# Kernel tuning notes

Hardware: AMD Instinct MI355X
Metric: run time of the kernel (lower is better)

## Reference

```python
import jax, jax.numpy as jnp
import numpy as np

B, N, C, O, K = 8, 1024, 64, 64, 3  # batch, nodes, in_c, out_c, Cheb order
EPS = 1e-12


def setup_inputs() -> dict:
    key = jax.random.key(0)
    ks = jax.random.split(key, 10)
    X_real = jax.random.normal(ks[0], (B, N, C), dtype=jnp.float32)
    X_imag = jax.random.normal(ks[1], (B, N, C), dtype=jnp.float32)
    L_real = jax.random.normal(ks[2], (B, K + 1, N, N), dtype=jnp.float32)
    L_imag = jax.random.normal(ks[3], (B, K + 1, N, N), dtype=jnp.float32)
    # Chebyshev weights: uniform(-stdv, stdv) then normalized to unit complex magnitude (as in __init__)
    stdv = 1.0 / np.sqrt(O)
    w_real = jax.random.uniform(ks[4], (K + 1, C, O), minval=-stdv, maxval=stdv, dtype=jnp.float32)
    w_imag = jax.random.uniform(ks[5], (K + 1, C, O), minval=-stdv, maxval=stdv, dtype=jnp.float32)
    mag = jnp.sqrt(w_real ** 2 + w_imag ** 2)
    w_real = w_real / mag
    w_imag = w_imag / mag
    # complex attention linear: maps 2*C -> 1
    a_stdv = 1.0 / np.sqrt(2 * C)
    attn_w_real = jax.random.uniform(ks[6], (2 * C,), minval=-a_stdv, maxval=a_stdv, dtype=jnp.float32)
    attn_w_imag = jax.random.uniform(ks[7], (2 * C,), minval=-a_stdv, maxval=a_stdv, dtype=jnp.float32)
    attn_b_real = jnp.zeros((1,), dtype=jnp.float32)
    attn_b_imag = jnp.zeros((1,), dtype=jnp.float32)
    # complex PReLU slopes (PyTorch PReLU default init 0.25)
    prelu_a_real = jnp.full((1,), 0.25, dtype=jnp.float32)
    prelu_a_imag = jnp.full((1,), 0.25, dtype=jnp.float32)
    return dict(X_real=X_real, X_imag=X_imag, L_real=L_real, L_imag=L_imag,
                w_real=w_real, w_imag=w_imag,
                attn_w_real=attn_w_real, attn_w_imag=attn_w_imag,
                attn_b_real=attn_b_real, attn_b_imag=attn_b_imag,
                prelu_a_real=prelu_a_real, prelu_a_imag=prelu_a_imag)


def reference(X_real, X_imag, L_real, L_imag, w_real, w_imag,
              attn_w_real, attn_w_imag, attn_b_real, attn_b_imag,
              prelu_a_real, prelu_a_imag):
    c = X_real.shape[-1]
    # --- attention scores: CVLinear on concat(x_i, x_j) decomposes into per-node terms ---
    Wr_i, Wr_j = attn_w_real[:c], attn_w_real[c:]
    Wi_i, Wi_j = attn_w_imag[:c], attn_w_imag[c:]
    sR_i = X_real @ Wr_i - X_imag @ Wi_i  # [B,N]
    sI_i = X_real @ Wi_i + X_imag @ Wr_i
    sR_j = X_real @ Wr_j - X_imag @ Wi_j
    sI_j = X_real @ Wi_j + X_imag @ Wr_j
    scores_r = sR_i[:, :, None] + sR_j[:, None, :] + attn_b_real  # [B,N,N]
    scores_i = sI_i[:, :, None] + sI_j[:, None, :] + attn_b_imag
    # --- complex PReLU (applied to real/imag separately) ---
    pr = jnp.where(scores_r >= 0, scores_r, prelu_a_real * scores_r)
    pi = jnp.where(scores_i >= 0, scores_i, prelu_a_imag * scores_i)
    # --- phase softmax over dim=1: softmax of magnitude, phase preserved ---
    mag = jnp.sqrt(pr ** 2 + pi ** 2)
    sm = jax.nn.softmax(mag, axis=1)
    scale = sm / (mag + EPS)
    ar = scale * pr  # [B,N,N] complex attention (real part)
    ai = scale * pi
    # --- modulate complex Laplacian stack [B,K+1,N,N] ---
    Lr = L_real * ar[:, None] - L_imag * ai[:, None]
    Li = L_real * ai[:, None] + L_imag * ar[:, None]
    # einsum 'bijk,bqjp->bijp' with q-size 1 == rowsum over k, then scale X per node j
    rowR = Lr.sum(-1)  # [B,K+1,N]
    rowI = Li.sum(-1)
    # complex (L-rowsum * X) @ W, summed over the K+1 terms (torch.sum dim=2 of stack)
    real = (jnp.einsum('bmj,bjc,mco->bjo', rowR, X_real, w_real)
            - jnp.einsum('bmj,bjc,mco->bjo', rowI, X_imag, w_imag))
    imag = (jnp.einsum('bmj,bjc,mco->bjo', rowI, X_real, w_real)
            + jnp.einsum('bmj,bjc,mco->bjo', rowR, X_imag, w_imag))
    return real, imag
```

## Files before the change

kernel.cpp:

```cpp
#include <hip/hip_runtime.h>

#define EPS_Q 1e-12f

typedef float nfloat4 __attribute__((ext_vector_type(4)));

__device__ __forceinline__ float wave_reduce_sum(float v) {
#pragma unroll
    for (int m = 32; m > 0; m >>= 1) v += __shfl_xor(v, m, 64);
    return v;
}

__global__ __launch_bounds__(256)
void k_scores(const float* __restrict__ Xr, const float* __restrict__ Xi,
              const float* __restrict__ awr, const float* __restrict__ awi,
              float* __restrict__ sRi, float* __restrict__ sIi,
              float* __restrict__ sRj, float* __restrict__ sIj) {
    const int lane = threadIdx.x & 63;
    const int row  = (blockIdx.x << 2) + (threadIdx.x >> 6);
    const float xr = Xr[row * 64 + lane];
    const float xi = Xi[row * 64 + lane];
    const float wri = awr[lane], wrj = awr[64 + lane];
    const float wii = awi[lane], wij = awi[64 + lane];
    float v0 = xr * wri - xi * wii;
    float v1 = xr * wii + xi * wri;
    float v2 = xr * wrj - xi * wij;
    float v3 = xr * wij + xi * wrj;
#pragma unroll
    for (int m = 32; m > 0; m >>= 1) {
        v0 += __shfl_xor(v0, m, 64);
        v1 += __shfl_xor(v1, m, 64);
        v2 += __shfl_xor(v2, m, 64);
        v3 += __shfl_xor(v3, m, 64);
    }
    if (lane == 0) {
        sRi[row] = v0;
        sIi[row] = v1;
        sRj[row] = v2;
        sIj[row] = v3;
    }
}

__global__ __launch_bounds__(256)
void k_softmax(const float* __restrict__ sRi, const float* __restrict__ sIi,
               const float* __restrict__ sRj, const float* __restrict__ sIj,
               float* __restrict__ cmax, float* __restrict__ cinv,
               const float* __restrict__ abr, const float* __restrict__ abi,
               const float* __restrict__ par_, const float* __restrict__ pai_) {
    const int lane = threadIdx.x & 63;
    const int row  = (blockIdx.x << 2) + (threadIdx.x >> 6);
    const int b    = row >> 10;
    const float br = abr[0], bi = abi[0], par = par_[0], pai = pai_[0];
    const float sRjv = sRj[row], sIjv = sIj[row];
    const float* pR = sRi + (b << 10);
    const float* pI = sIi + (b << 10);
    float mags[16];
    float mx = -3.4e38f;
#pragma unroll
    for (int t = 0; t < 16; ++t) {
        const int i = (t << 6) + lane;
        float sr = pR[i] + sRjv + br;
        float si = pI[i] + sIjv + bi;
        float pr = sr >= 0.f ? sr : par * sr;
        float pi = si >= 0.f ? si : pai * si;
        float mg = sqrtf(pr * pr + pi * pi);
        mags[t] = mg;
        mx = fmaxf(mx, mg);
    }
#pragma unroll
    for (int m = 32; m > 0; m >>= 1) mx = fmaxf(mx, __shfl_xor(mx, m, 64));
    float s = 0.f;
#pragma unroll
    for (int t = 0; t < 16; ++t) s += __expf(mags[t] - mx);
    s = wave_reduce_sum(s);
    if (lane == 0) {
        cmax[row] = mx;
        cinv[row] = 1.f / s;
    }
}

__device__ __forceinline__ void attn_coef(float srj, float sij, float mx, float is,
                                          float sri, float sii,
                                          float br, float bi, float par, float pai,
                                          float& ar, float& ai) {
    float sr = sri + srj + br;
    float si = sii + sij + bi;
    float pr = sr >= 0.f ? sr : par * sr;
    float pi = si >= 0.f ? si : pai * si;
    float mg = sqrtf(pr * pr + pi * pi);
    float sc = __expf(mg - mx) * is / (mg + EPS_Q);
    ar = sc * pr;
    ai = sc * pi;
}

__global__ __launch_bounds__(256)
void k_rowreduce(const float* __restrict__ Lr, const float* __restrict__ Li,
                 const float* __restrict__ sRi, const float* __restrict__ sIi,
                 const float* __restrict__ sRj, const float* __restrict__ sIj,
                 const float* __restrict__ cmax, const float* __restrict__ cinv,
                 const float* __restrict__ abr, const float* __restrict__ abi,
                 const float* __restrict__ par_, const float* __restrict__ pai_,
                 float* __restrict__ rowR, float* __restrict__ rowI) {
    const int lane = threadIdx.x & 63;
    const int wid  = (blockIdx.x << 2) + (threadIdx.x >> 6);
    const int b    = wid >> 10;
    const int i    = wid & 1023;
    const float br = abr[0], bi = abi[0], par = par_[0], pai = pai_[0];
    const float sri = sRi[wid], sii = sIi[wid];

    const float4* SRJ = (const float4*)(sRj + (b << 10));
    const float4* SIJ = (const float4*)(sIj + (b << 10));
    const float4* CMX = (const float4*)(cmax + (b << 10));
    const float4* CIV = (const float4*)(cinv + (b << 10));

    float arv[16], aiv[16];
#pragma unroll
    for (int t = 0; t < 4; ++t) {
        const int j4 = (t << 6) + lane;
        const float4 vr = SRJ[j4];
        const float4 vi = SIJ[j4];
        const float4 vm = CMX[j4];
        const float4 vs = CIV[j4];
        attn_coef(vr.x, vi.x, vm.x, vs.x, sri, sii, br, bi, par, pai,
                  arv[(t << 2) + 0], aiv[(t << 2) + 0]);
        attn_coef(vr.y, vi.y, vm.y, vs.y, sri, sii, br, bi, par, pai,
                  arv[(t << 2) + 1], aiv[(t << 2) + 1]);
        attn_coef(vr.z, vi.z, vm.z, vs.z, sri, sii, br, bi, par, pai,
                  arv[(t << 2) + 2], aiv[(t << 2) + 2]);
        attn_coef(vr.w, vi.w, vm.w, vs.w, sri, sii, br, bi, par, pai,
                  arv[(t << 2) + 3], aiv[(t << 2) + 3]);
    }

    const size_t rb = ((size_t)b << 22) + ((size_t)i << 10);
    const nfloat4* LR = (const nfloat4*)(Lr + rb);
    const nfloat4* LI = (const nfloat4*)(Li + rb);

    float accR[4] = {0.f, 0.f, 0.f, 0.f};
    float accI[4] = {0.f, 0.f, 0.f, 0.f};
#pragma unroll
    for (int m = 0; m < 4; ++m) {
        nfloat4 r[4], q[4];
#pragma unroll
        for (int t = 0; t < 4; ++t) {
            r[t] = __builtin_nontemporal_load(&LR[(m << 18) + (t << 6) + lane]);
            q[t] = __builtin_nontemporal_load(&LI[(m << 18) + (t << 6) + lane]);
        }
#pragma unroll
        for (int t = 0; t < 4; ++t) {
            accR[m] += r[t].x * arv[(t << 2) + 0] - q[t].x * aiv[(t << 2) + 0];
            accI[m] += r[t].x * aiv[(t << 2) + 0] + q[t].x * arv[(t << 2) + 0];
            accR[m] += r[t].y * arv[(t << 2) + 1] - q[t].y * aiv[(t << 2) + 1];
            accI[m] += r[t].y * aiv[(t << 2) + 1] + q[t].y * arv[(t << 2) + 1];
            accR[m] += r[t].z * arv[(t << 2) + 2] - q[t].z * aiv[(t << 2) + 2];
            accI[m] += r[t].z * aiv[(t << 2) + 2] + q[t].z * arv[(t << 2) + 2];
            accR[m] += r[t].w * arv[(t << 2) + 3] - q[t].w * aiv[(t << 2) + 3];
            accI[m] += r[t].w * aiv[(t << 2) + 3] + q[t].w * arv[(t << 2) + 3];
        }
    }

#pragma unroll
    for (int m = 0; m < 4; ++m) {
        float aR = accR[m], aI = accI[m];
#pragma unroll
        for (int s = 32; s > 0; s >>= 1) {
            aR += __shfl_xor(aR, s, 64);
            aI += __shfl_xor(aI, s, 64);
        }
        if (lane == 0) {
            rowR[((b << 2) + m) * 1024 + i] = aR;
            rowI[((b << 2) + m) * 1024 + i] = aI;
        }
    }
}

__global__ __launch_bounds__(256)
void k_output(const float* __restrict__ Xr, const float* __restrict__ Xi,
              const float* __restrict__ wr, const float* __restrict__ wi,
              const float* __restrict__ rowR, const float* __restrict__ rowI,
              float* __restrict__ out) {
    __shared__ float lxr[16][64];
    __shared__ float lxi[16][64];
    const int tid = threadIdx.x;
    const int rb  = blockIdx.x << 4;
    {
        const float4* s0 = (const float4*)(Xr + (size_t)rb * 64);
        const float4* s1 = (const float4*)(Xi + (size_t)rb * 64);
        ((float4*)&lxr[0][0])[tid] = s0[tid];
        ((float4*)&lxi[0][0])[tid] = s1[tid];
    }
    __syncthreads();
    const int wave = tid >> 6, lane = tid & 63;
    const int r0 = wave << 2;
    float u[4][4], v[4][4];
#pragma unroll
    for (int r = 0; r < 4; ++r)
#pragma unroll
        for (int m = 0; m < 4; ++m) { u[r][m] = 0.f; v[r][m] = 0.f; }
    for (int c = 0; c < 64; ++c) {
        float wrv[4], wiv[4];
#pragma unroll
        for (int m = 0; m < 4; ++m) {
            wrv[m] = wr[((m << 6) + c) * 64 + lane];
            wiv[m] = wi[((m << 6) + c) * 64 + lane];
        }
#pragma unroll
        for (int r = 0; r < 4; ++r) {
            const float xr = lxr[r0 + r][c];
            const float xi = lxi[r0 + r][c];
#pragma unroll
            for (int m = 0; m < 4; ++m) {
                u[r][m] += xr * wrv[m];
                v[r][m] += xi * wiv[m];
            }
        }
    }
#pragma unroll
    for (int r = 0; r < 4; ++r) {
        const int row = rb + r0 + r;
        const int b = row >> 10, j = row & 1023;
        float re = 0.f, im = 0.f;
#pragma unroll
        for (int m = 0; m < 4; ++m) {
            const float rr = rowR[(b << 12) + (m << 10) + j];
            const float ri = rowI[(b << 12) + (m << 10) + j];
            re += rr * u[r][m] - ri * v[r][m];
            im += ri * u[r][m] + rr * v[r][m];
        }
        out[(size_t)row * 64 + lane] = re;
        out[524288 + (size_t)row * 64 + lane] = im;
    }
}

extern "C" void kernel_launch(void* const* d_in, const int* in_sizes, int n_in,
                              void* d_out, int out_size, void* d_ws, size_t ws_size,
                              hipStream_t stream) {
    const float* Xr  = (const float*)d_in[0];
    const float* Xi  = (const float*)d_in[1];
    const float* Lr  = (const float*)d_in[2];
    const float* Li  = (const float*)d_in[3];
    const float* wr  = (const float*)d_in[4];
    const float* wi  = (const float*)d_in[5];
    const float* awr = (const float*)d_in[6];
    const float* awi = (const float*)d_in[7];
    const float* abr = (const float*)d_in[8];
    const float* abi = (const float*)d_in[9];
    const float* par = (const float*)d_in[10];
    const float* pai = (const float*)d_in[11];
    float* out = (float*)d_out;

    float* ws   = (float*)d_ws;
    float* sRi  = ws;
    float* sIi  = ws + 8192;
    float* sRj  = ws + 16384;
    float* sIj  = ws + 24576;
    float* cmax = ws + 32768;
    float* cinv = ws + 40960;
    float* rowR = ws + 49152;
    float* rowI = ws + 81920;

    k_scores   <<<dim3(2048), dim3(256), 0, stream>>>(Xr, Xi, awr, awi, sRi, sIi, sRj, sIj);
    k_softmax  <<<dim3(2048), dim3(256), 0, stream>>>(sRi, sIi, sRj, sIj, cmax, cinv,
                                                      abr, abi, par, pai);
    k_rowreduce<<<dim3(2048), dim3(256), 0, stream>>>(Lr, Li, sRi, sIi, sRj, sIj, cmax, cinv,
                                                      abr, abi, par, pai, rowR, rowI);
    k_output   <<<dim3(512),  dim3(256), 0, stream>>>(Xr, Xi, wr, wi, rowR, rowI, out);
}
```

Measured before the change: 320.3 us.

## Fuse output projection into row-reduce kernel and double-buffer Laplacian loads

Merges the per-node X@W projection and the complex combine into the Laplacian row-reduction kernel, so the separate output kernel and the rowR/rowI workspace round-trip go away. Each wave computes one Chebyshev order's projection for the block's 4 rows using lane shuffles and exchanges the results through shared memory. The L loads are also reordered into two alternating register buffers so the next order's load is issued before the current one's FMAs. In exchange, each block now re-reads W and X, and a __syncthreads is added inside the bandwidth-bound streaming kernel.

```diff
diff --git a/kernel.cpp b/kernel.cpp
--- a/kernel.cpp
+++ b/kernel.cpp
@@ -92,16 +92,45 @@
     ai = sc * pi;
 }
 
+#define FMA_BURST(m, R, Q)                                              \
+    {                                                                   \
+        _Pragma("unroll")                                               \
+        for (int t = 0; t < 4; ++t) {                                   \
+            accR[m] += R[t].x * arv[(t << 2) + 0] - Q[t].x * aiv[(t << 2) + 0]; \
+            accI[m] += R[t].x * aiv[(t << 2) + 0] + Q[t].x * arv[(t << 2) + 0]; \
+            accR[m] += R[t].y * arv[(t << 2) + 1] - Q[t].y * aiv[(t << 2) + 1]; \
+            accI[m] += R[t].y * aiv[(t << 2) + 1] + Q[t].y * arv[(t << 2) + 1]; \
+            accR[m] += R[t].z * arv[(t << 2) + 2] - Q[t].z * aiv[(t << 2) + 2]; \
+            accI[m] += R[t].z * aiv[(t << 2) + 2] + Q[t].z * arv[(t << 2) + 2]; \
+            accR[m] += R[t].w * arv[(t << 2) + 3] - Q[t].w * aiv[(t << 2) + 3]; \
+            accI[m] += R[t].w * aiv[(t << 2) + 3] + Q[t].w * arv[(t << 2) + 3]; \
+        }                                                               \
+    }
+
+#define LOAD_BURST(m, R, Q)                                             \
+    {                                                                   \
+        _Pragma("unroll")                                               \
+        for (int t = 0; t < 4; ++t) {                                   \
+            R[t] = __builtin_nontemporal_load(&LR[((m) << 18) + (t << 6) + lane]); \
+            Q[t] = __builtin_nontemporal_load(&LI[((m) << 18) + (t << 6) + lane]); \
+        }                                                               \
+    }
+
 __global__ __launch_bounds__(256)
-void k_rowreduce(const float* __restrict__ Lr, const float* __restrict__ Li,
-                 const float* __restrict__ sRi, const float* __restrict__ sIi,
-                 const float* __restrict__ sRj, const float* __restrict__ sIj,
-                 const float* __restrict__ cmax, const float* __restrict__ cinv,
-                 const float* __restrict__ abr, const float* __restrict__ abi,
-                 const float* __restrict__ par_, const float* __restrict__ pai_,
-                 float* __restrict__ rowR, float* __restrict__ rowI) {
+void k_stream_out(const float* __restrict__ Lr, const float* __restrict__ Li,
+                  const float* __restrict__ sRi, const float* __restrict__ sIi,
+                  const float* __restrict__ sRj, const float* __restrict__ sIj,
+                  const float* __restrict__ cmax, const float* __restrict__ cinv,
+                  const float* __restrict__ abr, const float* __restrict__ abi,
+                  const float* __restrict__ par_, const float* __restrict__ pai_,
+                  const float* __restrict__ Xr, const float* __restrict__ Xi,
+                  const float* __restrict__ wr, const float* __restrict__ wi,
+                  float* __restrict__ out) {
+    __shared__ float luR[4][4][64];
+    __shared__ float luI[4][4][64];
     const int lane = threadIdx.x & 63;
-    const int wid  = (blockIdx.x << 2) + (threadIdx.x >> 6);
+    const int wave = threadIdx.x >> 6;
+    const int wid  = (blockIdx.x << 2) + wave;
     const int b    = wid >> 10;
     const int i    = wid & 1023;
     const float br = abr[0], bi = abi[0], par = par_[0], pai = pai_[0];
@@ -130,104 +159,66 @@
                   arv[(t << 2) + 3], aiv[(t << 2) + 3]);
     }
 
-    const size_t rb = ((size_t)b << 22) + ((size_t)i << 10);
-    const nfloat4* LR = (const nfloat4*)(Lr + rb);
-    const nfloat4* LI = (const nfloat4*)(Li + rb);
+    const size_t base = ((size_t)b << 22) + ((size_t)i << 10);
+    const nfloat4* LR = (const nfloat4*)(Lr + base);
+    const nfloat4* LI = (const nfloat4*)(Li + base);
 
     float accR[4] = {0.f, 0.f, 0.f, 0.f};
     float accI[4] = {0.f, 0.f, 0.f, 0.f};
+    nfloat4 rA[4], qA[4], rB[4], qB[4];
+    LOAD_BURST(0, rA, qA);
+    LOAD_BURST(1, rB, qB);
+    FMA_BURST(0, rA, qA);
+    LOAD_BURST(2, rA, qA);
+    FMA_BURST(1, rB, qB);
+    LOAD_BURST(3, rB, qB);
+    FMA_BURST(2, rA, qA);
+    FMA_BURST(3, rB, qB);
+
 #pragma unroll
     for (int m = 0; m < 4; ++m) {
-        nfloat4 r[4], q[4];
-#pragma unroll
-        for (int t = 0; t < 4; ++t) {
-            r[t] = __builtin_nontemporal_load(&LR[(m << 18) + (t << 6) + lane]);
-            q[t] = __builtin_nontemporal_load(&LI[(m << 18) + (t << 6) + lane]);
+#pragma unroll
+        for (int s = 32; s > 0; s >>= 1) {
+            accR[m] += __shfl_xor(accR[m], s, 64);
+            accI[m] += __shfl_xor(accI[m], s, 64);
         }
-#pragma unroll
-        for (int t = 0; t < 4; ++t) {
-            accR[m] += r[t].x * arv[(t << 2) + 0] - q[t].x * aiv[(t << 2) + 0];
-            accI[m] += r[t].x * aiv[(t << 2) + 0] + q[t].x * arv[(t << 2) + 0];
-            accR[m] += r[t].y * arv[(t << 2) + 1] - q[t].y * aiv[(t << 2) + 1];
-            accI[m] += r[t].y * aiv[(t << 2) + 1] + q[t].y * arv[(t << 2) + 1];
-            accR[m] += r[t].z * arv[(t << 2) + 2] - q[t].z * aiv[(t << 2) + 2];
-            accI[m] += r[t].z * aiv[(t << 2) + 2] + q[t].z * arv[(t << 2) + 2];
-            accR[m] += r[t].w * arv[(t << 2) + 3] - q[t].w * aiv[(t << 2) + 3];
-            accI[m] += r[t].w * aiv[(t << 2) + 3] + q[t].w * arv[(t << 2) + 3];
+    }
+
+    const int row0 = blockIdx.x << 2;
+    float xrv[4], xiv[4];
+#pragma unroll
+    for (int r = 0; r < 4; ++r) {
+        xrv[r] = Xr[(size_t)(row0 + r) * 64 + lane];
+        xiv[r] = Xi[(size_t)(row0 + r) * 64 + lane];
+    }
+    float u[4] = {0.f, 0.f, 0.f, 0.f};
+    float v[4] = {0.f, 0.f, 0.f, 0.f};
+#pragma unroll 4
+    for (int c = 0; c < 64; ++c) {
+        const float wrv = wr[(((wave << 6) + c) << 6) + lane];
+        const float wiv = wi[(((wave << 6) + c) << 6) + lane];
+#pragma unroll
+        for (int r = 0; r < 4; ++r) {
+            u[r] += __shfl(xrv[r], c, 64) * wrv;
+            v[r] += __shfl(xiv[r], c, 64) * wiv;
         }
     }
-
+#pragma unroll
+    for (int r = 0; r < 4; ++r) {
+        luR[wave][r][lane] = u[r];
+        luI[wave][r][lane] = v[r];
+    }
+    __syncthreads();
+    float re = 0.f, im = 0.f;
 #pragma unroll
     for (int m = 0; m < 4; ++m) {
-        float aR = accR[m], aI = accI[m];
-#pragma unroll
-        for (int s = 32; s > 0; s >>= 1) {
-            aR += __shfl_xor(aR, s, 64);
-            aI += __shfl_xor(aI, s, 64);
-        }
-        if (lane == 0) {
-            rowR[((b << 2) + m) * 1024 + i] = aR;
-            rowI[((b << 2) + m) * 1024 + i] = aI;
-        }
-    }
-}
-
-__global__ __launch_bounds__(256)
-void k_output(const float* __restrict__ Xr, const float* __restrict__ Xi,
-              const float* __restrict__ wr, const float* __restrict__ wi,
-              const float* __restrict__ rowR, const float* __restrict__ rowI,
-              float* __restrict__ out) {
-    __shared__ float lxr[16][64];
-    __shared__ float lxi[16][64];
-    const int tid = threadIdx.x;
-    const int rb  = blockIdx.x << 4;
-    {
-        const float4* s0 = (const float4*)(Xr + (size_t)rb * 64);
-        const float4* s1 = (const float4*)(Xi + (size_t)rb * 64);
-        ((float4*)&lxr[0][0])[tid] = s0[tid];
-        ((float4*)&lxi[0][0])[tid] = s1[tid];
-    }
-    __syncthreads();
-    const int wave = tid >> 6, lane = tid & 63;
-    const int r0 = wave << 2;
-    float u[4][4], v[4][4];
-#pragma unroll
-    for (int r = 0; r < 4; ++r)
-#pragma unroll
-        for (int m = 0; m < 4; ++m) { u[r][m] = 0.f; v[r][m] = 0.f; }
-    for (int c = 0; c < 64; ++c) {
-        float wrv[4], wiv[4];
-#pragma unroll
-        for (int m = 0; m < 4; ++m) {
-            wrv[m] = wr[((m << 6) + c) * 64 + lane];
-            wiv[m] = wi[((m << 6) + c) * 64 + lane];
-        }
-#pragma unroll
-        for (int r = 0; r < 4; ++r) {
-            const float xr = lxr[r0 + r][c];
-            const float xi = lxi[r0 + r][c];
-#pragma unroll
-            for (int m = 0; m < 4; ++m) {
-                u[r][m] += xr * wrv[m];
-                v[r][m] += xi * wiv[m];
-            }
-        }
-    }
-#pragma unroll
-    for (int r = 0; r < 4; ++r) {
-        const int row = rb + r0 + r;
-        const int b = row >> 10, j = row & 1023;
-        float re = 0.f, im = 0.f;
-#pragma unroll
-        for (int m = 0; m < 4; ++m) {
-            const float rr = rowR[(b << 12) + (m << 10) + j];
-            const float ri = rowI[(b << 12) + (m << 10) + j];
-            re += rr * u[r][m] - ri * v[r][m];
-            im += ri * u[r][m] + rr * v[r][m];
-        }
-        out[(size_t)row * 64 + lane] = re;
-        out[524288 + (size_t)row * 64 + lane] = im;
-    }
+        const float um = luR[m][wave][lane];
+        const float vm = luI[m][wave][lane];
+        re += accR[m] * um - accI[m] * vm;
+        im += accI[m] * um + accR[m] * vm;
+    }
+    out[(size_t)wid * 64 + lane] = re;
+    out[524288 + (size_t)wid * 64 + lane] = im;
 }
 
 extern "C" void kernel_launch(void* const* d_in, const int* in_sizes, int n_in,
@@ -254,13 +245,11 @@
     float* sIj  = ws + 24576;
     float* cmax = ws + 32768;
     float* cinv = ws + 40960;
-    float* rowR = ws + 49152;
-    float* rowI = ws + 81920;
-
-    k_scores   <<<dim3(2048), dim3(256), 0, stream>>>(Xr, Xi, awr, awi, sRi, sIi, sRj, sIj);
-    k_softmax  <<<dim3(2048), dim3(256), 0, stream>>>(sRi, sIi, sRj, sIj, cmax, cinv,
-                                                      abr, abi, par, pai);
-    k_rowreduce<<<dim3(2048), dim3(256), 0, stream>>>(Lr, Li, sRi, sIi, sRj, sIj, cmax, cinv,
-                                                      abr, abi, par, pai, rowR, rowI);
-    k_output   <<<dim3(512),  dim3(256), 0, stream>>>(Xr, Xi, wr, wi, rowR, rowI, out);
-}
+
+    k_scores    <<<dim3(2048), dim3(256), 0, stream>>>(Xr, Xi, awr, awi, sRi, sIi, sRj, sIj);
+    k_softmax   <<<dim3(2048), dim3(256), 0, stream>>>(sRi, sIi, sRj, sIj, cmax, cinv,
+                                                       abr, abi, par, pai);
+    k_stream_out<<<dim3(2048), dim3(256), 0, stream>>>(Lr, Li, sRi, sIi, sRj, sIj, cmax, cinv,
+                                                       abr, abi, par, pai,
+                                                       Xr, Xi, wr, wi, out);
+}
```

Result: faster. 309.5 us (-3.4%).
